# Kernel tuning notes

Hardware: AMD Instinct MI355X
Metric: run time of the kernel (lower is better)

## Reference

```python
import jax, jax.numpy as jnp
import numpy as np

B, T, D, H = 2, 4096, 768, 12
HD = D // H  # head_dim = 64


def setup_inputs() -> dict:
    key = jax.random.key(0)
    ks = jax.random.split(key, 6)
    s = 0.02
    return {
        "x": jax.random.normal(ks[0], (B, T, D), dtype=jnp.float32),
        "Wq": jax.random.normal(ks[1], (D, D), dtype=jnp.float32) * s,
        "Wk": jax.random.normal(ks[2], (D, D), dtype=jnp.float32) * s,
        "Wv": jax.random.normal(ks[3], (D, D), dtype=jnp.float32) * s,
        "Wo": jax.random.normal(ks[4], (D, D), dtype=jnp.float32) * s,
        "bo": jnp.zeros((D,), dtype=jnp.float32),
    }


def reference(x, Wq, Wk, Wv, Wo, bo):
    b, t, d = x.shape
    # QKV projections (no bias), reshape to [B, H, T, HD]
    def heads(w):
        return (x @ w.T).reshape(b, t, H, HD).transpose(0, 2, 1, 3)
    q, k, v = heads(Wq), heads(Wk), heads(Wv)
    scores = jnp.einsum("bhqd,bhkd->bhqk", q, k)  # [B,H,T,T]
    causal = jnp.tril(jnp.ones((t, t), dtype=bool))
    scores = jnp.where(causal, scores, -jnp.inf)
    attn = jax.nn.softmax(scores / jnp.sqrt(jnp.float32(HD)), axis=-1)
    ctx = jnp.einsum("bhqk,bhkd->bhqd", attn, v)  # [B,H,T,HD]
    ctx = ctx.transpose(0, 2, 1, 3).reshape(b, t, d)
    return ctx @ Wo.T + bo
```

## Files before the change

### kernel.cpp

```cpp
#include <hip/hip_runtime.h>
#include <hip/hip_bf16.h>
#include <cstdint>
#include <cstddef>

#define B_  2
#define T_  4096
#define D_  768
#define H_  12
#define HD_ 64
#define M_  (B_*T_)

#define SCL 0.18033688f

typedef __bf16 bf16x8 __attribute__((ext_vector_type(8)));
typedef float  f32x4  __attribute__((ext_vector_type(4)));
using bf16 = __hip_bfloat16;

__device__ inline float fexp2(float x) {
  float r; asm("v_exp_f32 %0, %1" : "=v"(r) : "v"(x)); return r;
}
__device__ inline uint32_t fu(float x) { union { float f; uint32_t u; } c; c.f = x; return c.u; }
__device__ inline uint32_t pktr(float a, float b) {
  return __builtin_amdgcn_perm(fu(b), fu(a), 0x07060302);
}
#define GLD16(g, l) __builtin_amdgcn_global_load_lds( \
    (const __attribute__((address_space(1))) uint32_t*)(const void*)(g), \
    (__attribute__((address_space(3))) uint32_t*)(void*)(l), 16, 0, 0)

__global__ void cvt_all(const float* __restrict__ x,
                        const float* __restrict__ w0, const float* __restrict__ w1,
                        const float* __restrict__ w2, const float* __restrict__ w3,
                        bf16* __restrict__ xd,
                        bf16* __restrict__ d0, bf16* __restrict__ d1,
                        bf16* __restrict__ d2, bf16* __restrict__ d3) {
  const float* s; bf16* d; int n4;
  switch (blockIdx.y) {
    case 0: s = x;  d = xd; n4 = M_ * D_ / 4; break;
    case 1: s = w0; d = d0; n4 = D_ * D_ / 4; break;
    case 2: s = w1; d = d1; n4 = D_ * D_ / 4; break;
    case 3: s = w2; d = d2; n4 = D_ * D_ / 4; break;
    default: s = w3; d = d3; n4 = D_ * D_ / 4; break;
  }
  int i = blockIdx.x * blockDim.x + threadIdx.x;
  if (i < n4) {
    float4 v = ((const float4*)s)[i];
    union { bf16 o[4]; uint2 u; } pk;
    pk.o[0] = __float2bfloat16(v.x); pk.o[1] = __float2bfloat16(v.y);
    pk.o[2] = __float2bfloat16(v.z); pk.o[3] = __float2bfloat16(v.w);
    *(uint2*)(d + 4 * (size_t)i) = pk.u;
  }
}

__global__ __launch_bounds__(256) void gemm_qkv(const bf16* __restrict__ A,
                                                const bf16* __restrict__ W0,
                                                const bf16* __restrict__ W1,
                                                const bf16* __restrict__ W2,
                                                bf16* __restrict__ O0,
                                                bf16* __restrict__ O1,
                                                bf16* __restrict__ O2t) {
  __shared__ bf16 As[2][4096];
  __shared__ bf16 Bs[2][4096];
  const int z = blockIdx.z;
  const char* Bw = (const char*)((z == 0) ? W0 : ((z == 1) ? W1 : W2));
  const char* Ap = (const char*)A;
  const int t  = threadIdx.x;
  const int m0 = blockIdx.y * 128;
  const int n0 = blockIdx.x * 128;
  const int w = t >> 6, lane = t & 63;
  const int wm = (w >> 1) * 64, wn = (w & 1) * 64;
  const int mi = lane & 15, qd = lane >> 4;

  int aoff[2], boff[2];
  #pragma unroll
  for (int i = 0; i < 2; ++i) {
    int L = i * 256 + t;
    int row = L >> 2, sl = L & 3, c = sl ^ (row & 3);
    aoff[i] = (m0 + row) * 1536 + c * 16;
    boff[i] = (n0 + row) * 1536 + c * 16;
  }
  const int fsw = (qd ^ (mi & 3)) * 8;

  f32x4 acc[4][4] = {};

  #pragma unroll
  for (int i = 0; i < 2; ++i) {
    GLD16(Ap + aoff[i], &As[0][i * 2048 + w * 512]);
    GLD16(Bw + boff[i], &Bs[0][i * 2048 + w * 512]);
  }

  for (int kk = 0; kk < 24; ++kk) {
    __syncthreads();
    const int par = kk & 1;
    if (kk + 1 < 24) {
      const int np = par ^ 1, kb = (kk + 1) * 64;
      #pragma unroll
      for (int i = 0; i < 2; ++i) {
        GLD16(Ap + aoff[i] + kb, &As[np][i * 2048 + w * 512]);
        GLD16(Bw + boff[i] + kb, &Bs[np][i * 2048 + w * 512]);
      }
    }
    bf16x8 af[4], bfr[4];
    #pragma unroll
    for (int mt = 0; mt < 4; ++mt)
      af[mt] = *(const bf16x8*)&As[par][(wm + mt * 16 + mi) * 32 + fsw];
    #pragma unroll
    for (int nt = 0; nt < 4; ++nt)
      bfr[nt] = *(const bf16x8*)&Bs[par][(wn + nt * 16 + mi) * 32 + fsw];
    #pragma unroll
    for (int mt = 0; mt < 4; ++mt)
      #pragma unroll
      for (int nt = 0; nt < 4; ++nt)
        acc[mt][nt] = __builtin_amdgcn_mfma_f32_16x16x32_bf16(af[mt], bfr[nt], acc[mt][nt], 0, 0, 0);
  }

  const float scl = (z == 1) ? SCL : 1.0f;
  bf16* Ob = (z == 0) ? O0 : O1;
  #pragma unroll
  for (int mt = 0; mt < 4; ++mt) {
    #pragma unroll
    for (int nt = 0; nt < 4; ++nt) {
      int gr0 = m0 + wm + mt * 16 + qd * 4;
      int gc  = n0 + wn + nt * 16 + mi;
      if (z == 2) {
        union { bf16 o[4]; uint2 u; } pk;
        #pragma unroll
        for (int r = 0; r < 4; ++r) pk.o[r] = __float2bfloat16(acc[mt][nt][r]);
        int bb = gr0 >> 12, tt = gr0 & 4095;
        *(uint2*)(O2t + (size_t)bb * 768 * 4096 + (size_t)gc * 4096 + tt) = pk.u;
      } else {
        #pragma unroll
        for (int r = 0; r < 4; ++r)
          Ob[(size_t)(gr0 + r) * 768 + gc] = __float2bfloat16(acc[mt][nt][r] * scl);
      }
    }
  }
}

__global__ __launch_bounds__(256) void gemm_out(const bf16* __restrict__ A,
                                                const bf16* __restrict__ Bw0,
                                                float* __restrict__ Cf,
                                                const float* __restrict__ bias) {
  __shared__ bf16 As[2][4096];
  __shared__ bf16 Bs[2][4096];
  const char* Ap = (const char*)A;
  const char* Bw = (const char*)Bw0;
  const int t  = threadIdx.x;
  const int m0 = blockIdx.y * 128;
  const int n0 = blockIdx.x * 128;
  const int w = t >> 6, lane = t & 63;
  const int wm = (w >> 1) * 64, wn = (w & 1) * 64;
  const int mi = lane & 15, qd = lane >> 4;

  int aoff[2], boff[2];
  #pragma unroll
  for (int i = 0; i < 2; ++i) {
    int L = i * 256 + t;
    int row = L >> 2, sl = L & 3, c = sl ^ (row & 3);
    aoff[i] = (m0 + row) * 1536 + c * 16;
    boff[i] = (n0 + row) * 1536 + c * 16;
  }
  const int fsw = (qd ^ (mi & 3)) * 8;

  f32x4 acc[4][4] = {};

  #pragma unroll
  for (int i = 0; i < 2; ++i) {
    GLD16(Ap + aoff[i], &As[0][i * 2048 + w * 512]);
    GLD16(Bw + boff[i], &Bs[0][i * 2048 + w * 512]);
  }

  for (int kk = 0; kk < 24; ++kk) {
    __syncthreads();
    const int par = kk & 1;
    if (kk + 1 < 24) {
      const int np = par ^ 1, kb = (kk + 1) * 64;
      #pragma unroll
      for (int i = 0; i < 2; ++i) {
        GLD16(Ap + aoff[i] + kb, &As[np][i * 2048 + w * 512]);
        GLD16(Bw + boff[i] + kb, &Bs[np][i * 2048 + w * 512]);
      }
    }
    bf16x8 af[4], bfr[4];
    #pragma unroll
    for (int mt = 0; mt < 4; ++mt)
      af[mt] = *(const bf16x8*)&As[par][(wm + mt * 16 + mi) * 32 + fsw];
    #pragma unroll
    for (int nt = 0; nt < 4; ++nt)
      bfr[nt] = *(const bf16x8*)&Bs[par][(wn + nt * 16 + mi) * 32 + fsw];
    #pragma unroll
    for (int mt = 0; mt < 4; ++mt)
      #pragma unroll
      for (int nt = 0; nt < 4; ++nt)
        acc[mt][nt] = __builtin_amdgcn_mfma_f32_16x16x32_bf16(af[mt], bfr[nt], acc[mt][nt], 0, 0, 0);
  }

  #pragma unroll
  for (int mt = 0; mt < 4; ++mt)
    #pragma unroll
    for (int nt = 0; nt < 4; ++nt) {
      int gr0 = m0 + wm + mt * 16 + qd * 4;
      int gc  = n0 + wn + nt * 16 + mi;
      #pragma unroll
      for (int r = 0; r < 4; ++r)
        Cf[(size_t)(gr0 + r) * 768 + gc] = acc[mt][nt][r] + bias[gc];
    }
}

__global__ __launch_bounds__(256) void flash_attn(const bf16* __restrict__ Q,
                                                  const bf16* __restrict__ K,
                                                  const bf16* __restrict__ Vt,
                                                  bf16* __restrict__ ctx) {
  __shared__ bf16 Ks[2][4096];
  __shared__ bf16 Vs[2][4096];
  __shared__ bf16 Pt[4][32 * 72];
  const int t = threadIdx.x;
  const int w = t >> 6, lane = t & 63;
  const int mi = lane & 15, qd = lane >> 4;
  const int bh   = blockIdx.x % 24;
  const int qrev = blockIdx.x / 24;
  const int q0 = T_ - 128 - qrev * 128;
  const int b = bh / H_, h = bh % H_;
  const size_t bTD = (size_t)b * T_ * D_;
  const char* Kp = (const char*)(K  + bTD + (size_t)h * HD_);
  const char* Vp = (const char*)(Vt + (size_t)b * D_ * T_ + (size_t)h * HD_ * T_);
  const int qwmin = q0 + w * 32;

  int vkoff[2], vvoff[2];
  #pragma unroll
  for (int i = 0; i < 2; ++i) {
    int s  = i * 64 + lane;
    int rl = s >> 3, cs = s & 7;
    int c  = cs ^ (rl & 7);
    vkoff[i] = (w * 16 + rl) * 1536 + c * 16;
    vvoff[i] = (w * 16 + rl) * 8192 + c * 16;
  }

  int fidx[4][2];
  #pragma unroll
  for (int jt = 0; jt < 4; ++jt)
    #pragma unroll
    for (int kt = 0; kt < 2; ++kt)
      fidx[jt][kt] = (jt * 16 + mi) * 64 + (((kt * 4 + qd) ^ (mi & 7)) * 8);

  bf16x8 qf[2][2];
  const bf16* Qp = Q + bTD + (size_t)h * HD_;
  #pragma unroll
  for (int qt = 0; qt < 2; ++qt)
    #pragma unroll
    for (int kt = 0; kt < 2; ++kt)
      qf[qt][kt] = *(const bf16x8*)(Qp + (size_t)(qwmin + qt * 16 + mi) * D_ + kt * 32 + qd * 8);

  f32x4 oacc[4][2] = {};
  float lst[2] = {0.f, 0.f};

  const int ntiles = q0 / 64 + 2;

  #pragma unroll
  for (int i = 0; i < 2; ++i) {
    GLD16(Kp + vkoff[i], &Ks[0][w * 1024 + i * 512]);
    GLD16(Vp + vvoff[i], &Vs[0][w * 1024 + i * 512]);
  }

  for (int tt = 0; tt < ntiles; ++tt) {
    __syncthreads();
    const int par = tt & 1;
    if (tt + 1 < ntiles) {
      const size_t j1 = (size_t)(tt + 1) * 64;
      const int np = par ^ 1;
      #pragma unroll
      for (int i = 0; i < 2; ++i) {
        GLD16(Kp + vkoff[i] + j1 * 1536, &Ks[np][w * 1024 + i * 512]);
        GLD16(Vp + vvoff[i] + j1 * 2,    &Vs[np][w * 1024 + i * 512]);
      }
    }
    const int j0 = tt * 64;
    if (j0 > qwmin + 31) continue;

    f32x4 sacc[4][2] = {};
    #pragma unroll
    for (int jt = 0; jt < 4; ++jt)
      #pragma unroll
      for (int kt = 0; kt < 2; ++kt) {
        bf16x8 kf = *(const bf16x8*)&Ks[par][fidx[jt][kt]];
        #pragma unroll
        for (int qt = 0; qt < 2; ++qt)
          sacc[jt][qt] = __builtin_amdgcn_mfma_f32_16x16x32_bf16(kf, qf[qt][kt], sacc[jt][qt], 0, 0, 0);
      }

    if (j0 + 63 > qwmin) {
      #pragma unroll
      for (int jt = 0; jt < 4; ++jt)
        #pragma unroll
        for (int qt = 0; qt < 2; ++qt) {
          int qg = qwmin + qt * 16 + mi;
          #pragma unroll
          for (int r = 0; r < 4; ++r) {
            int jg = j0 + jt * 16 + qd * 4 + r;
            if (jg > qg) sacc[jt][qt][r] = -1e30f;
          }
        }
    }

    #pragma unroll
    for (int jt = 0; jt < 4; ++jt)
      #pragma unroll
      for (int qt = 0; qt < 2; ++qt) {
        float p0 = fexp2(sacc[jt][qt][0]);
        float p1 = fexp2(sacc[jt][qt][1]);
        float p2 = fexp2(sacc[jt][qt][2]);
        float p3 = fexp2(sacc[jt][qt][3]);
        lst[qt] += (p0 + p1) + (p2 + p3);
        union { uint32_t u[2]; uint64_t d; } pw;
        pw.u[0] = pktr(p0, p1);
        pw.u[1] = pktr(p2, p3);
        *(uint64_t*)&Pt[w][(qt * 16 + mi) * 72 + jt * 16 + qd * 4] = pw.d;
      }

    bf16x8 vf[4][2];
    #pragma unroll
    for (int dt = 0; dt < 4; ++dt)
      #pragma unroll
      for (int kt = 0; kt < 2; ++kt)
        vf[dt][kt] = *(const bf16x8*)&Vs[par][fidx[dt][kt]];

    asm volatile("s_waitcnt lgkmcnt(0)" ::: "memory");

    #pragma unroll
    for (int ktp = 0; ktp < 2; ++ktp)
      #pragma unroll
      for (int qt = 0; qt < 2; ++qt) {
        bf16x8 pf = *(const bf16x8*)&Pt[w][(qt * 16 + mi) * 72 + ktp * 32 + qd * 8];
        #pragma unroll
        for (int dt = 0; dt < 4; ++dt)
          oacc[dt][qt] = __builtin_amdgcn_mfma_f32_16x16x32_bf16(vf[dt][ktp], pf, oacc[dt][qt], 0, 0, 0);
      }
  }

  #pragma unroll
  for (int qt = 0; qt < 2; ++qt) {
    float l = lst[qt];
    l += __shfl_xor(l, 16);
    l += __shfl_xor(l, 32);
    float inv = __builtin_amdgcn_rcpf(l);
    int qg = qwmin + qt * 16 + mi;
    bf16* cp = ctx + bTD + (size_t)qg * D_ + h * HD_ + qd * 4;
    #pragma unroll
    for (int dt = 0; dt < 4; ++dt) {
      union { bf16 o[4]; uint2 u; } pko;
      #pragma unroll
      for (int r = 0; r < 4; ++r) pko.o[r] = __float2bfloat16(oacc[dt][qt][r] * inv);
      *(uint2*)(cp + dt * 16) = pko.u;
    }
  }
}

extern "C" void kernel_launch(void* const* d_in, const int* in_sizes, int n_in,
                              void* d_out, int out_size, void* d_ws, size_t ws_size,
                              hipStream_t stream) {
  const float* x  = (const float*)d_in[0];
  const float* Wq = (const float*)d_in[1];
  const float* Wk = (const float*)d_in[2];
  const float* Wv = (const float*)d_in[3];
  const float* Wo = (const float*)d_in[4];
  const float* bo = (const float*)d_in[5];
  float* out = (float*)d_out;

  char* ws = (char*)d_ws;
  const size_t SZ  = (size_t)M_ * D_ * 2;
  const size_t WSZ = (size_t)D_ * D_ * 2;
  bf16* xb   = (bf16*)(ws);
  bf16* Qb   = (bf16*)(ws + 1 * SZ);
  bf16* Kb   = (bf16*)(ws + 2 * SZ);
  bf16* Vtg  = (bf16*)(ws + 3 * SZ);
  bf16* ctxb = (bf16*)(ws + 4 * SZ);
  bf16* Wqb  = (bf16*)(ws + 5 * SZ);
  bf16* Wkb  = (bf16*)(ws + 5 * SZ + 1 * WSZ);
  bf16* Wvb  = (bf16*)(ws + 5 * SZ + 2 * WSZ);
  bf16* Wob  = (bf16*)(ws + 5 * SZ + 3 * WSZ);

  dim3 gcv(M_ * D_ / 4 / 256, 5);
  cvt_all<<<gcv, 256, 0, stream>>>(x, Wq, Wk, Wv, Wo, xb, Wqb, Wkb, Wvb, Wob);

  dim3 gq(D_ / 128, M_ / 128, 3);
  gemm_qkv<<<gq, 256, 0, stream>>>(xb, Wqb, Wkb, Wvb, Qb, Kb, Vtg);

  flash_attn<<<(T_ / 128) * B_ * H_, 256, 0, stream>>>(Qb, Kb, Vtg, ctxb);

  dim3 gg(D_ / 128, M_ / 128);
  gemm_out<<<gg, 256, 0, stream>>>(ctxb, Wob, out, bo);
}
```

Measured before the change: 266.0 us.

## Pre-swizzle bf16 operands into MFMA fragment order and drop LDS staging in GEMMs

The conversion kernel now writes x and the weights in a tiled layout that matches the 16x16x32 MFMA fragment, so each lane can load its 8-element fragment straight from global memory. Both projection GEMMs stop staging tiles in shared memory. They double-buffer fragments in registers and drop the per-iteration barriers. The cost is that operands shared across waves are now fetched separately by each wave through the cache hierarchy, which raises global and L2 traffic. gemm_out's A operand (ctx) is read row-major with strided 16-byte loads.

```diff
diff --git a/kernel.cpp b/kernel.cpp
--- a/kernel.cpp
+++ b/kernel.cpp
@@ -27,28 +27,32 @@
     (const __attribute__((address_space(1))) uint32_t*)(const void*)(g), \
     (__attribute__((address_space(3))) uint32_t*)(void*)(l), 16, 0, 0)
 
-__global__ void cvt_all(const float* __restrict__ x,
-                        const float* __restrict__ w0, const float* __restrict__ w1,
-                        const float* __restrict__ w2, const float* __restrict__ w3,
-                        bf16* __restrict__ xd,
-                        bf16* __restrict__ d0, bf16* __restrict__ d1,
-                        bf16* __restrict__ d2, bf16* __restrict__ d3) {
-  const float* s; bf16* d; int n4;
+__global__ void cvt_frag(const float* __restrict__ x,
+                         const float* __restrict__ w0, const float* __restrict__ w1,
+                         const float* __restrict__ w2, const float* __restrict__ w3,
+                         bf16* __restrict__ xd,
+                         bf16* __restrict__ d0, bf16* __restrict__ d1,
+                         bf16* __restrict__ d2, bf16* __restrict__ d3) {
+  const float* s; bf16* d; int n8;
   switch (blockIdx.y) {
-    case 0: s = x;  d = xd; n4 = M_ * D_ / 4; break;
-    case 1: s = w0; d = d0; n4 = D_ * D_ / 4; break;
-    case 2: s = w1; d = d1; n4 = D_ * D_ / 4; break;
-    case 3: s = w2; d = d2; n4 = D_ * D_ / 4; break;
-    default: s = w3; d = d3; n4 = D_ * D_ / 4; break;
+    case 0: s = x;  d = xd; n8 = M_ * D_ / 8; break;
+    case 1: s = w0; d = d0; n8 = D_ * D_ / 8; break;
+    case 2: s = w1; d = d1; n8 = D_ * D_ / 8; break;
+    case 3: s = w2; d = d2; n8 = D_ * D_ / 8; break;
+    default: s = w3; d = d3; n8 = D_ * D_ / 8; break;
   }
   int i = blockIdx.x * blockDim.x + threadIdx.x;
-  if (i < n4) {
-    float4 v = ((const float4*)s)[i];
-    union { bf16 o[4]; uint2 u; } pk;
-    pk.o[0] = __float2bfloat16(v.x); pk.o[1] = __float2bfloat16(v.y);
-    pk.o[2] = __float2bfloat16(v.z); pk.o[3] = __float2bfloat16(v.w);
-    *(uint2*)(d + 4 * (size_t)i) = pk.u;
-  }
+  if (i >= n8) return;
+  int row = i / 96, kg = i % 96;
+  float4 v0 = ((const float4*)s)[i * 2];
+  float4 v1 = ((const float4*)s)[i * 2 + 1];
+  union { bf16 o[8]; uint4 u; } pk;
+  pk.o[0] = __float2bfloat16(v0.x); pk.o[1] = __float2bfloat16(v0.y);
+  pk.o[2] = __float2bfloat16(v0.z); pk.o[3] = __float2bfloat16(v0.w);
+  pk.o[4] = __float2bfloat16(v1.x); pk.o[5] = __float2bfloat16(v1.y);
+  pk.o[6] = __float2bfloat16(v1.z); pk.o[7] = __float2bfloat16(v1.w);
+  size_t off = ((size_t)((row >> 4) * 24 + (kg >> 2)) * 64 + (kg & 3) * 16 + (row & 15)) * 8;
+  *(uint4*)(d + off) = pk.u;
 }
 
 __global__ __launch_bounds__(256) void gemm_qkv(const bf16* __restrict__ A,
@@ -58,59 +62,46 @@
                                                 bf16* __restrict__ O0,
                                                 bf16* __restrict__ O1,
                                                 bf16* __restrict__ O2t) {
-  __shared__ bf16 As[2][4096];
-  __shared__ bf16 Bs[2][4096];
   const int z = blockIdx.z;
-  const char* Bw = (const char*)((z == 0) ? W0 : ((z == 1) ? W1 : W2));
-  const char* Ap = (const char*)A;
-  const int t  = threadIdx.x;
-  const int m0 = blockIdx.y * 128;
-  const int n0 = blockIdx.x * 128;
+  const bf16* Bw = (z == 0) ? W0 : ((z == 1) ? W1 : W2);
+  const int t = threadIdx.x;
   const int w = t >> 6, lane = t & 63;
   const int wm = (w >> 1) * 64, wn = (w & 1) * 64;
   const int mi = lane & 15, qd = lane >> 4;
-
-  int aoff[2], boff[2];
-  #pragma unroll
-  for (int i = 0; i < 2; ++i) {
-    int L = i * 256 + t;
-    int row = L >> 2, sl = L & 3, c = sl ^ (row & 3);
-    aoff[i] = (m0 + row) * 1536 + c * 16;
-    boff[i] = (n0 + row) * 1536 + c * 16;
-  }
-  const int fsw = (qd ^ (mi & 3)) * 8;
+  const int m0 = blockIdx.y * 128, n0 = blockIdx.x * 128;
+
+  const bf16* ap[4]; const bf16* bp[4];
+  #pragma unroll
+  for (int i = 0; i < 4; ++i) {
+    int mtg = (m0 + wm) / 16 + i;
+    int ntg = (n0 + wn) / 16 + i;
+    ap[i] = A  + (size_t)mtg * 24 * 512 + lane * 8;
+    bp[i] = Bw + (size_t)ntg * 24 * 512 + lane * 8;
+  }
 
   f32x4 acc[4][4] = {};
-
-  #pragma unroll
-  for (int i = 0; i < 2; ++i) {
-    GLD16(Ap + aoff[i], &As[0][i * 2048 + w * 512]);
-    GLD16(Bw + boff[i], &Bs[0][i * 2048 + w * 512]);
-  }
-
+  bf16x8 af[2][4], bf[2][4];
+  #pragma unroll
+  for (int i = 0; i < 4; ++i) {
+    af[0][i] = *(const bf16x8*)(ap[i]);
+    bf[0][i] = *(const bf16x8*)(bp[i]);
+  }
+
+  #pragma unroll 2
   for (int kk = 0; kk < 24; ++kk) {
-    __syncthreads();
-    const int par = kk & 1;
+    const int c = kk & 1;
     if (kk + 1 < 24) {
-      const int np = par ^ 1, kb = (kk + 1) * 64;
-      #pragma unroll
-      for (int i = 0; i < 2; ++i) {
-        GLD16(Ap + aoff[i] + kb, &As[np][i * 2048 + w * 512]);
-        GLD16(Bw + boff[i] + kb, &Bs[np][i * 2048 + w * 512]);
-      }
-    }
-    bf16x8 af[4], bfr[4];
+      #pragma unroll
+      for (int i = 0; i < 4; ++i) {
+        af[c ^ 1][i] = *(const bf16x8*)(ap[i] + (kk + 1) * 512);
+        bf[c ^ 1][i] = *(const bf16x8*)(bp[i] + (kk + 1) * 512);
+      }
+    }
     #pragma unroll
     for (int mt = 0; mt < 4; ++mt)
-      af[mt] = *(const bf16x8*)&As[par][(wm + mt * 16 + mi) * 32 + fsw];
-    #pragma unroll
-    for (int nt = 0; nt < 4; ++nt)
-      bfr[nt] = *(const bf16x8*)&Bs[par][(wn + nt * 16 + mi) * 32 + fsw];
-    #pragma unroll
-    for (int mt = 0; mt < 4; ++mt)
       #pragma unroll
       for (int nt = 0; nt < 4; ++nt)
-        acc[mt][nt] = __builtin_amdgcn_mfma_f32_16x16x32_bf16(af[mt], bfr[nt], acc[mt][nt], 0, 0, 0);
+        acc[mt][nt] = __builtin_amdgcn_mfma_f32_16x16x32_bf16(af[c][mt], bf[c][nt], acc[mt][nt], 0, 0, 0);
   }
 
   const float scl = (z == 1) ? SCL : 1.0f;
@@ -137,61 +128,46 @@
 }
 
 __global__ __launch_bounds__(256) void gemm_out(const bf16* __restrict__ A,
-                                                const bf16* __restrict__ Bw0,
+                                                const bf16* __restrict__ Bw,
                                                 float* __restrict__ Cf,
                                                 const float* __restrict__ bias) {
-  __shared__ bf16 As[2][4096];
-  __shared__ bf16 Bs[2][4096];
-  const char* Ap = (const char*)A;
-  const char* Bw = (const char*)Bw0;
-  const int t  = threadIdx.x;
-  const int m0 = blockIdx.y * 128;
-  const int n0 = blockIdx.x * 128;
+  const int t = threadIdx.x;
   const int w = t >> 6, lane = t & 63;
   const int wm = (w >> 1) * 64, wn = (w & 1) * 64;
   const int mi = lane & 15, qd = lane >> 4;
-
-  int aoff[2], boff[2];
-  #pragma unroll
-  for (int i = 0; i < 2; ++i) {
-    int L = i * 256 + t;
-    int row = L >> 2, sl = L & 3, c = sl ^ (row & 3);
-    aoff[i] = (m0 + row) * 1536 + c * 16;
-    boff[i] = (n0 + row) * 1536 + c * 16;
-  }
-  const int fsw = (qd ^ (mi & 3)) * 8;
+  const int m0 = blockIdx.y * 128, n0 = blockIdx.x * 128;
+
+  const bf16* ap[4]; const bf16* bp[4];
+  #pragma unroll
+  for (int i = 0; i < 4; ++i) {
+    ap[i] = A + (size_t)(m0 + wm + i * 16 + mi) * 768 + qd * 8;
+    int ntg = (n0 + wn) / 16 + i;
+    bp[i] = Bw + (size_t)ntg * 24 * 512 + lane * 8;
+  }
 
   f32x4 acc[4][4] = {};
-
-  #pragma unroll
-  for (int i = 0; i < 2; ++i) {
-    GLD16(Ap + aoff[i], &As[0][i * 2048 + w * 512]);
-    GLD16(Bw + boff[i], &Bs[0][i * 2048 + w * 512]);
-  }
-
+  bf16x8 af[2][4], bf[2][4];
+  #pragma unroll
+  for (int i = 0; i < 4; ++i) {
+    af[0][i] = *(const bf16x8*)(ap[i]);
+    bf[0][i] = *(const bf16x8*)(bp[i]);
+  }
+
+  #pragma unroll 2
   for (int kk = 0; kk < 24; ++kk) {
-    __syncthreads();
-    const int par = kk & 1;
+    const int c = kk & 1;
     if (kk + 1 < 24) {
-      const int np = par ^ 1, kb = (kk + 1) * 64;
-      #pragma unroll
-      for (int i = 0; i < 2; ++i) {
-        GLD16(Ap + aoff[i] + kb, &As[np][i * 2048 + w * 512]);
-        GLD16(Bw + boff[i] + kb, &Bs[np][i * 2048 + w * 512]);
-      }
-    }
-    bf16x8 af[4], bfr[4];
+      #pragma unroll
+      for (int i = 0; i < 4; ++i) {
+        af[c ^ 1][i] = *(const bf16x8*)(ap[i] + (kk + 1) * 32);
+        bf[c ^ 1][i] = *(const bf16x8*)(bp[i] + (kk + 1) * 512);
+      }
+    }
     #pragma unroll
     for (int mt = 0; mt < 4; ++mt)
-      af[mt] = *(const bf16x8*)&As[par][(wm + mt * 16 + mi) * 32 + fsw];
-    #pragma unroll
-    for (int nt = 0; nt < 4; ++nt)
-      bfr[nt] = *(const bf16x8*)&Bs[par][(wn + nt * 16 + mi) * 32 + fsw];
-    #pragma unroll
-    for (int mt = 0; mt < 4; ++mt)
       #pragma unroll
       for (int nt = 0; nt < 4; ++nt)
-        acc[mt][nt] = __builtin_amdgcn_mfma_f32_16x16x32_bf16(af[mt], bfr[nt], acc[mt][nt], 0, 0, 0);
+        acc[mt][nt] = __builtin_amdgcn_mfma_f32_16x16x32_bf16(af[c][mt], bf[c][nt], acc[mt][nt], 0, 0, 0);
   }
 
   #pragma unroll
@@ -378,8 +354,8 @@
   bf16* Wvb  = (bf16*)(ws + 5 * SZ + 2 * WSZ);
   bf16* Wob  = (bf16*)(ws + 5 * SZ + 3 * WSZ);
 
-  dim3 gcv(M_ * D_ / 4 / 256, 5);
-  cvt_all<<<gcv, 256, 0, stream>>>(x, Wq, Wk, Wv, Wo, xb, Wqb, Wkb, Wvb, Wob);
+  dim3 gcv(M_ * D_ / 8 / 256, 5);
+  cvt_frag<<<gcv, 256, 0, stream>>>(x, Wq, Wk, Wv, Wo, xb, Wqb, Wkb, Wvb, Wob);
 
   dim3 gq(D_ / 128, M_ / 128, 3);
   gemm_qkv<<<gq, 256, 0, stream>>>(xb, Wqb, Wkb, Wvb, Qb, Kb, Vtg);
```

After: 289.1 us. 1.09x slower.
